# Kernel tuning notes

Measured on AMD Instinct MI355X. Metric: run time of the kernel, lower is better.

## Reference

```python
import jax, jax.numpy as jnp
import numpy as np

N_EMBD = 1024
N_HEAD = 16
HEAD_DIM = N_EMBD // N_HEAD


def setup_inputs() -> dict:
    key = jax.random.key(0)
    k1, k2, k3, k4, k5 = jax.random.split(key, 5)
    B, T, C = 4, 2048, N_EMBD
    s = 1.0 / np.sqrt(C)
    return {
        "x": jax.random.normal(k1, (B, T, C), dtype=jnp.float32),
        "W_attn": jax.random.normal(k2, (C, 3 * C), dtype=jnp.float32) * s,
        "b_attn": jnp.zeros((3 * C,), dtype=jnp.float32),
        "W_proj": jax.random.normal(k3, (C, C), dtype=jnp.float32) * s,
        "b_proj": jnp.zeros((C,), dtype=jnp.float32),
    }


def reference(x, W_attn, b_attn, W_proj, b_proj):
    B, T, C = x.shape
    H, D = N_HEAD, HEAD_DIM
    # fused QKV projection
    qkv = x @ W_attn + b_attn                       # [B,T,3C]
    q, k, v = jnp.split(qkv, 3, axis=2)
    q = q.reshape(B, T, H, D).transpose(0, 2, 1, 3)  # [B,H,T,D]
    k = k.reshape(B, T, H, D).transpose(0, 2, 1, 3)
    v = v.reshape(B, T, H, D).transpose(0, 2, 1, 3)
    # causal scaled dot-product attention
    scale = 1.0 / jnp.sqrt(jnp.asarray(D, dtype=x.dtype))
    scores = jnp.einsum('bhqd,bhkd->bhqk', q, k) * scale  # [B,H,T,T]
    causal = jnp.tril(jnp.ones((T, T), dtype=bool))
    scores = jnp.where(causal[None, None], scores, jnp.finfo(x.dtype).min)
    attn = jax.nn.softmax(scores, axis=-1)
    y = jnp.einsum('bhqk,bhkd->bhqd', attn, v)      # [B,H,T,D]
    y = y.transpose(0, 2, 1, 3).reshape(B, T, C)
    return y @ W_proj + b_proj
```

## Files before the change

kernel.cpp:

```cpp
#include <hip/hip_runtime.h>
#include <hip/hip_bf16.h>
#include <cstdint>

#define B_ 4
#define T_ 2048
#define C_ 1024
#define H_ 16
#define D_ 64
#define M_ (B_*T_)
#define N3 (3*C_)

typedef __bf16 bf16;
typedef __bf16 bf16x8 __attribute__((ext_vector_type(8)));
typedef __bf16 bf16x4 __attribute__((ext_vector_type(4)));
typedef float  floatx4 __attribute__((ext_vector_type(4)));

__device__ __forceinline__ void gl_lds16(const bf16* g, bf16* l) {
  __builtin_amdgcn_global_load_lds(
      (__attribute__((address_space(1))) void*)(void*)g,
      (__attribute__((address_space(3))) void*)(void*)l,
      16, 0, 0);
}

__device__ __forceinline__ uint32_t pack_bf16_trunc(float lo, float hi) {
  union { float f; uint32_t u; } a, b;
  a.f = lo; b.f = hi;
  return (a.u >> 16) | (b.u & 0xffff0000u);
}

__global__ void cast_to_bf16(const float* __restrict__ in, bf16* __restrict__ out, int n) {
  int i = (blockIdx.x * blockDim.x + threadIdx.x) * 4;
  if (i < n) {
    const float4 f = *(const float4*)(in + i);
    bf16x4 o;
    o.x = (bf16)f.x; o.y = (bf16)f.y; o.z = (bf16)f.z; o.w = (bf16)f.w;
    *(bf16x4*)(out + i) = o;
  }
}

__global__ void transpose_cast(const float* __restrict__ in, bf16* __restrict__ out,
                               int R, int C) {
  __shared__ float tile[32][33];
  int r0 = blockIdx.y * 32, c0 = blockIdx.x * 32;
  int tx = threadIdx.x & 31, ty = threadIdx.x >> 5;
  #pragma unroll
  for (int j = 0; j < 32; j += 8)
    tile[ty + j][tx] = in[(size_t)(r0 + ty + j) * C + c0 + tx];
  __syncthreads();
  #pragma unroll
  for (int j = 0; j < 32; j += 8)
    out[(size_t)(c0 + ty + j) * R + r0 + tx] = (bf16)tile[tx][ty + j];
}

__global__ __launch_bounds__(256)
void transpose_v(const bf16* __restrict__ in, bf16* __restrict__ out) {
  __shared__ __attribute__((aligned(16))) bf16 tileN[64 * 64];
  const int tid = threadIdx.x;
  const int bh = blockIdx.z;
  const int t0 = blockIdx.x * 64;
  const int sk = tid >> 2, scc = tid & 3;
  {
    const bf16* p = in + ((size_t)bh * T_ + t0 + sk) * D_ + scc * 16;
    const bf16x8 r0 = *(const bf16x8*)p;
    const bf16x8 r1 = *(const bf16x8*)(p + 8);
    *(bf16x8*)(tileN + sk * 64 + ((2 * scc)     ^ (sk & 7)) * 8) = r0;
    *(bf16x8*)(tileN + sk * 64 + ((2 * scc + 1) ^ (sk & 7)) * 8) = r1;
  }
  __syncthreads();
  const int tc = (tid & 7) * 8;
  #pragma unroll
  for (int half = 0; half < 2; half++) {
    const int d = (tid >> 3) + half * 32;
    bf16x8 o;
    #pragma unroll
    for (int j = 0; j < 8; j++) {
      const int slot = tc + j;
      const int row = 16 * (slot & 3) + (slot >> 2);
      o[j] = tileN[row * 64 + (((d >> 3) ^ (row & 7)) * 8) + (d & 7)];
    }
    *(bf16x8*)(out + ((size_t)bh * D_ + d) * T_ + t0 + tc) = o;
  }
}

template<int MODE>
__global__ __launch_bounds__(256)
void gemm_bt(const bf16* __restrict__ A, const bf16* __restrict__ Bt,
             const float* __restrict__ bias, float* __restrict__ out,
             bf16* __restrict__ qo, bf16* __restrict__ ko, bf16* __restrict__ vo,
             int M, int N, int K)
{
  __shared__ __attribute__((aligned(16))) bf16 As[128 * 32];
  __shared__ __attribute__((aligned(16))) bf16 Bs[128 * 32];

  const int tid  = threadIdx.x;
  const int w    = tid >> 6;
  const int lane = tid & 63;
  const int quad = lane >> 4;
  const int l16  = lane & 15;
  const int wm   = w & 1, wn = w >> 1;
  const int m0   = blockIdx.y * 128, n0 = blockIdx.x * 128;

  floatx4 acc[4][4] = {};

  const int lrow = lane >> 2;
  const int lk   = (lane & 3) * 8;

  const bf16* aptr = A  + (size_t)(m0 + w * 32 + lrow) * K + lk;
  const bf16* bptr = Bt + (size_t)(n0 + w * 32 + lrow) * K + lk;
  bf16* asl = As + w * 1024;
  bf16* bsl = Bs + w * 1024;

  for (int k0 = 0; k0 < K; k0 += 32) {
    gl_lds16(aptr,          asl);
    gl_lds16(aptr + 16 * K, asl + 512);
    gl_lds16(bptr,          bsl);
    gl_lds16(bptr + 16 * K, bsl + 512);
    aptr += 32; bptr += 32;
    __syncthreads();

    bf16x8 af[4], bfb[4];
    #pragma unroll
    for (int i = 0; i < 4; i++)
      af[i] = *(const bf16x8*)(As + (wm * 64 + i * 16 + l16) * 32 + quad * 8);
    #pragma unroll
    for (int i = 0; i < 4; i++)
      bfb[i] = *(const bf16x8*)(Bs + (wn * 64 + i * 16 + l16) * 32 + quad * 8);
    #pragma unroll
    for (int mi = 0; mi < 4; mi++)
      #pragma unroll
      for (int ni = 0; ni < 4; ni++)
        acc[mi][ni] = __builtin_amdgcn_mfma_f32_16x16x32_bf16(af[mi], bfb[ni], acc[mi][ni], 0, 0, 0);
    __syncthreads();
  }

  #pragma unroll
  for (int mi = 0; mi < 4; mi++) {
    #pragma unroll
    for (int ni = 0; ni < 4; ni++) {
      const int col = n0 + wn * 64 + ni * 16 + l16;
      const float bv = bias[col];
      #pragma unroll
      for (int r = 0; r < 4; r++) {
        const int row = m0 + wm * 64 + mi * 16 + quad * 4 + r;
        const float val = acc[mi][ni][r] + bv;
        if (MODE == 0) {
          const int b = row >> 11, t = row & 2047;
          const int s = col >> 10, c = col & 1023;
          const int h = c >> 6,  d = c & 63;
          bf16* dst = (s == 0) ? qo : (s == 1) ? ko : vo;
          dst[((size_t)(b * H_ + h) * T_ + t) * D_ + d] = (bf16)val;
        } else {
          out[(size_t)row * N + col] = val;
        }
      }
    }
  }
}

__global__ __launch_bounds__(256)
void attn_kernel(const bf16* __restrict__ Q, const bf16* __restrict__ Kp,
                 const bf16* __restrict__ Vtp, bf16* __restrict__ Y)
{
  __shared__ __attribute__((aligned(16))) bf16 Ks[2][64 * 72];
  __shared__ __attribute__((aligned(16))) bf16 Vs[2][64 * 72];
  __shared__ __attribute__((aligned(16))) bf16 Ps[4][16 * 72];

  const int tid  = threadIdx.x;
  const int w    = tid >> 6, lane = tid & 63;
  const int quad = lane >> 4, l16 = lane & 15;
  const int bh = blockIdx.x;
  const int b = bh >> 4, h = bh & 15;
  const int qt = 15 - (int)blockIdx.y;
  const int q0 = qt * 128;
  const int nch = 2 * qt + 2;

  const int sk = tid >> 2;
  const int sc = (tid & 3) * 16;

  const float SC = 0.125f * 1.44269504088896f;

  bf16x8 qf[2][2];
  #pragma unroll
  for (int mt = 0; mt < 2; mt++) {
    const bf16* qp = Q + ((size_t)bh * T_ + q0 + mt * 64 + w * 16 + l16) * D_ + quad * 8;
    qf[mt][0] = *(const bf16x8*)qp;
    qf[mt][1] = *(const bf16x8*)(qp + 32);
  }

  floatx4 o[2][4] = {};
  float l_r[2][4] = {};

  const bf16* kpp = Kp  + (size_t)bh * T_ * D_ + (size_t)sk * D_ + sc;
  const bf16* vpp = Vtp + (size_t)bh * D_ * T_ + (size_t)sk * T_ + sc;

  {
    const bf16x8 k0 = *(const bf16x8*)kpp, k1 = *(const bf16x8*)(kpp + 8);
    const bf16x8 v0 = *(const bf16x8*)vpp, v1 = *(const bf16x8*)(vpp + 8);
    bf16* kd = Ks[0] + sk * 72 + sc;
    *(bf16x8*)kd = k0; *(bf16x8*)(kd + 8) = k1;
    bf16* vd = Vs[0] + sk * 72 + sc;
    *(bf16x8*)vd = v0; *(bf16x8*)(vd + 8) = v1;
    kpp += 64 * D_; vpp += 64;
  }
  __syncthreads();

  #pragma unroll 1
  for (int c = 0; c < nch; c++) {
    const int cur = c & 1;

    bf16x8 nk0, nk1, nv0, nv1;
    const bool have = (c + 1 < nch);
    if (have) {
      nk0 = *(const bf16x8*)kpp; nk1 = *(const bf16x8*)(kpp + 8);
      nv0 = *(const bf16x8*)vpp; nv1 = *(const bf16x8*)(vpp + 8);
      kpp += 64 * D_; vpp += 64;
    }

    const bf16* KsC = Ks[cur];
    const bf16* VsC = Vs[cur];
    const int kv0 = c * 64;
    const bool act0 = (c < nch - 1);

    floatx4 s[2][4];
    #pragma unroll
    for (int nt = 0; nt < 4; nt++) {
      const bf16x8 kf0 = *(const bf16x8*)(KsC + (nt * 16 + l16) * 72 + quad * 8);
      const bf16x8 kf1 = *(const bf16x8*)(KsC + (nt * 16 + l16) * 72 + 32 + quad * 8);
      if (act0) {
        floatx4 z = {};
        z = __builtin_amdgcn_mfma_f32_16x16x32_bf16(qf[0][0], kf0, z, 0, 0, 0);
        s[0][nt] = __builtin_amdgcn_mfma_f32_16x16x32_bf16(qf[0][1], kf1, z, 0, 0, 0);
      }
      floatx4 z = {};
      z = __builtin_amdgcn_mfma_f32_16x16x32_bf16(qf[1][0], kf0, z, 0, 0, 0);
      s[1][nt] = __builtin_amdgcn_mfma_f32_16x16x32_bf16(qf[1][1], kf1, z, 0, 0, 0);
    }

    bf16x8 vfr[4][2];
    #pragma unroll
    for (int nt = 0; nt < 4; nt++) {
      vfr[nt][0] = *(const bf16x8*)(VsC + (nt * 16 + l16) * 72 + quad * 8);
      vfr[nt][1] = *(const bf16x8*)(VsC + (nt * 16 + l16) * 72 + 32 + quad * 8);
    }

    #pragma unroll
    for (int mt = 0; mt < 2; mt++) {
      if (mt == 0 && !act0) continue;
      const bool diag = (c == 2 * qt + mt);
      #pragma unroll
      for (int r = 0; r < 4; r++) {
        const int qrow = q0 + mt * 64 + w * 16 + quad * 4 + r;
        float x0 = s[mt][0][r], x1 = s[mt][1][r], x2 = s[mt][2][r], x3 = s[mt][3][r];
        if (diag) {
          if (kv0      + l16 > qrow) x0 = -1e30f;
          if (kv0 + 16 + l16 > qrow) x1 = -1e30f;
          if (kv0 + 32 + l16 > qrow) x2 = -1e30f;
          if (kv0 + 48 + l16 > qrow) x3 = -1e30f;
        }
        const float e0 = __builtin_amdgcn_exp2f(fmaf(x0, SC, -8.f));
        const float e1 = __builtin_amdgcn_exp2f(fmaf(x1, SC, -8.f));
        const float e2 = __builtin_amdgcn_exp2f(fmaf(x2, SC, -8.f));
        const float e3 = __builtin_amdgcn_exp2f(fmaf(x3, SC, -8.f));
        l_r[mt][r] += (e0 + e1) + (e2 + e3);
        uint2 pk;
        pk.x = pack_bf16_trunc(e0, e1);
        pk.y = pack_bf16_trunc(e2, e3);
        *(uint2*)(&Ps[w][(quad * 4 + r) * 72 + l16 * 4]) = pk;
      }
      const bf16x8 pf0 = *(const bf16x8*)(&Ps[w][l16 * 72 + quad * 8]);
      const bf16x8 pf1 = *(const bf16x8*)(&Ps[w][l16 * 72 + 32 + quad * 8]);
      #pragma unroll
      for (int nt = 0; nt < 4; nt++) {
        o[mt][nt] = __builtin_amdgcn_mfma_f32_16x16x32_bf16(pf0, vfr[nt][0], o[mt][nt], 0, 0, 0);
        o[mt][nt] = __builtin_amdgcn_mfma_f32_16x16x32_bf16(pf1, vfr[nt][1], o[mt][nt], 0, 0, 0);
      }
    }

    if (have) {
      bf16* kd = Ks[cur ^ 1] + sk * 72 + sc;
      *(bf16x8*)kd = nk0; *(bf16x8*)(kd + 8) = nk1;
      bf16* vd = Vs[cur ^ 1] + sk * 72 + sc;
      *(bf16x8*)vd = nv0; *(bf16x8*)(vd + 8) = nv1;
    }
    __syncthreads();
  }

  #pragma unroll
  for (int mt = 0; mt < 2; mt++) {
    #pragma unroll
    for (int r = 0; r < 4; r++) {
      float ls = l_r[mt][r];
      ls += __shfl_xor(ls, 1);
      ls += __shfl_xor(ls, 2);
      ls += __shfl_xor(ls, 4);
      ls += __shfl_xor(ls, 8);
      const float inv = 1.f / ls;
      const int t = q0 + mt * 64 + w * 16 + quad * 4 + r;
      #pragma unroll
      for (int nt = 0; nt < 4; nt++)
        Y[((size_t)b * T_ + t) * C_ + h * D_ + nt * 16 + l16] = (bf16)(o[mt][nt][r] * inv);
    }
  }
}

extern "C" void kernel_launch(void* const* d_in, const int* in_sizes, int n_in,
                              void* d_out, int out_size, void* d_ws, size_t ws_size,
                              hipStream_t stream)
{
  const float* x      = (const float*)d_in[0];
  const float* W_attn = (const float*)d_in[1];
  const float* b_attn = (const float*)d_in[2];
  const float* W_proj = (const float*)d_in[3];
  const float* b_proj = (const float*)d_in[4];
  float* out = (float*)d_out;

  bf16* xb  = (bf16*)d_ws;
  bf16* wat = xb  + (size_t)M_ * C_;
  bf16* wpt = wat + (size_t)N3 * C_;
  bf16* qb  = wpt + (size_t)C_ * C_;
  bf16* kb  = qb  + (size_t)M_ * C_;
  bf16* vb  = kb  + (size_t)M_ * C_;
  bf16* yb  = vb  + (size_t)M_ * C_;
  bf16* vtb = xb;

  cast_to_bf16<<<dim3(M_ * C_ / 1024), 256, 0, stream>>>(x, xb, M_ * C_);
  transpose_cast<<<dim3(N3 / 32, C_ / 32), 256, 0, stream>>>(W_attn, wat, C_, N3);
  transpose_cast<<<dim3(C_ / 32, C_ / 32), 256, 0, stream>>>(W_proj, wpt, C_, C_);
  gemm_bt<0><<<dim3(N3 / 128, M_ / 128), 256, 0, stream>>>(
      xb, wat, b_attn, nullptr, qb, kb, vb, M_, N3, C_);
  transpose_v<<<dim3(T_ / 64, 1, B_ * H_), 256, 0, stream>>>(vb, vtb);
  attn_kernel<<<dim3(B_ * H_, 16), 256, 0, stream>>>(qb, kb, vtb, yb);
  gemm_bt<1><<<dim3(C_ / 128, M_ / 128), 256, 0, stream>>>(
      yb, wpt, b_proj, out, nullptr, nullptr, nullptr, M_, C_, C_);
}
```

Measured before the change: 268.5 us.

## Fuse V transpose into QKV GEMM epilogue and vectorize GEMM output stores

The MFMA operand order is swapped so each lane's accumulator holds four consecutive output columns. The QKV and projection epilogues can then write bf16x4 and float4 vectors instead of scattered scalars. For the V slice, the epilogue writes directly into the permuted transposed layout that attention expects, so the separate transpose_v kernel and its round trip through memory go away. The cost is more complex epilogue indexing that must exactly match the token permutation the attention kernel assumes.

```diff
diff --git a/kernel.cpp b/kernel.cpp
--- a/kernel.cpp
+++ b/kernel.cpp
@@ -52,41 +52,11 @@
     out[(size_t)(c0 + ty + j) * R + r0 + tx] = (bf16)tile[tx][ty + j];
 }
 
-__global__ __launch_bounds__(256)
-void transpose_v(const bf16* __restrict__ in, bf16* __restrict__ out) {
-  __shared__ __attribute__((aligned(16))) bf16 tileN[64 * 64];
-  const int tid = threadIdx.x;
-  const int bh = blockIdx.z;
-  const int t0 = blockIdx.x * 64;
-  const int sk = tid >> 2, scc = tid & 3;
-  {
-    const bf16* p = in + ((size_t)bh * T_ + t0 + sk) * D_ + scc * 16;
-    const bf16x8 r0 = *(const bf16x8*)p;
-    const bf16x8 r1 = *(const bf16x8*)(p + 8);
-    *(bf16x8*)(tileN + sk * 64 + ((2 * scc)     ^ (sk & 7)) * 8) = r0;
-    *(bf16x8*)(tileN + sk * 64 + ((2 * scc + 1) ^ (sk & 7)) * 8) = r1;
-  }
-  __syncthreads();
-  const int tc = (tid & 7) * 8;
-  #pragma unroll
-  for (int half = 0; half < 2; half++) {
-    const int d = (tid >> 3) + half * 32;
-    bf16x8 o;
-    #pragma unroll
-    for (int j = 0; j < 8; j++) {
-      const int slot = tc + j;
-      const int row = 16 * (slot & 3) + (slot >> 2);
-      o[j] = tileN[row * 64 + (((d >> 3) ^ (row & 7)) * 8) + (d & 7)];
-    }
-    *(bf16x8*)(out + ((size_t)bh * D_ + d) * T_ + t0 + tc) = o;
-  }
-}
-
 template<int MODE>
 __global__ __launch_bounds__(256)
 void gemm_bt(const bf16* __restrict__ A, const bf16* __restrict__ Bt,
              const float* __restrict__ bias, float* __restrict__ out,
-             bf16* __restrict__ qo, bf16* __restrict__ ko, bf16* __restrict__ vo,
+             bf16* __restrict__ qo, bf16* __restrict__ ko, bf16* __restrict__ vtp,
              int M, int N, int K)
 {
   __shared__ __attribute__((aligned(16))) bf16 As[128 * 32];
@@ -126,32 +96,63 @@
     for (int i = 0; i < 4; i++)
       bfb[i] = *(const bf16x8*)(Bs + (wn * 64 + i * 16 + l16) * 32 + quad * 8);
     #pragma unroll
-    for (int mi = 0; mi < 4; mi++)
-      #pragma unroll
-      for (int ni = 0; ni < 4; ni++)
-        acc[mi][ni] = __builtin_amdgcn_mfma_f32_16x16x32_bf16(af[mi], bfb[ni], acc[mi][ni], 0, 0, 0);
+    for (int ni = 0; ni < 4; ni++)
+      #pragma unroll
+      for (int mi = 0; mi < 4; mi++)
+        acc[ni][mi] = __builtin_amdgcn_mfma_f32_16x16x32_bf16(bfb[ni], af[mi], acc[ni][mi], 0, 0, 0);
     __syncthreads();
   }
 
-  #pragma unroll
-  for (int mi = 0; mi < 4; mi++) {
+  if (MODE == 0) {
+    const int s   = n0 >> 10;
+    const int h   = ((n0 & 1023) >> 6) + wn;
+    const int b   = m0 >> 11;
+    const int t0w = (m0 & 2047) + wm * 64;
+    const size_t bh = (size_t)(b * H_ + h);
+    if (s < 2) {
+      bf16* dst = (s == 0) ? qo : ko;
+      #pragma unroll
+      for (int ni = 0; ni < 4; ni++) {
+        const float4 bv = *(const float4*)(bias + n0 + wn * 64 + ni * 16 + quad * 4);
+        #pragma unroll
+        for (int mi = 0; mi < 4; mi++) {
+          bf16x4 pv;
+          pv.x = (bf16)(acc[ni][mi][0] + bv.x);
+          pv.y = (bf16)(acc[ni][mi][1] + bv.y);
+          pv.z = (bf16)(acc[ni][mi][2] + bv.z);
+          pv.w = (bf16)(acc[ni][mi][3] + bv.w);
+          *(bf16x4*)(dst + (bh * T_ + t0w + mi * 16 + l16) * D_ + ni * 16 + quad * 4) = pv;
+        }
+      }
+    } else {
+      #pragma unroll
+      for (int ni = 0; ni < 4; ni++) {
+        const float4 bvv = *(const float4*)(bias + n0 + wn * 64 + ni * 16 + quad * 4);
+        const float bvr[4] = {bvv.x, bvv.y, bvv.z, bvv.w};
+        #pragma unroll
+        for (int r = 0; r < 4; r++) {
+          bf16x4 pv;
+          pv.x = (bf16)(acc[ni][0][r] + bvr[r]);
+          pv.y = (bf16)(acc[ni][1][r] + bvr[r]);
+          pv.z = (bf16)(acc[ni][2][r] + bvr[r]);
+          pv.w = (bf16)(acc[ni][3][r] + bvr[r]);
+          *(bf16x4*)(vtp + (bh * D_ + ni * 16 + quad * 4 + r) * T_ + t0w + 4 * l16) = pv;
+        }
+      }
+    }
+  } else {
     #pragma unroll
     for (int ni = 0; ni < 4; ni++) {
-      const int col = n0 + wn * 64 + ni * 16 + l16;
-      const float bv = bias[col];
-      #pragma unroll
-      for (int r = 0; r < 4; r++) {
-        const int row = m0 + wm * 64 + mi * 16 + quad * 4 + r;
-        const float val = acc[mi][ni][r] + bv;
-        if (MODE == 0) {
-          const int b = row >> 11, t = row & 2047;
-          const int s = col >> 10, c = col & 1023;
-          const int h = c >> 6,  d = c & 63;
-          bf16* dst = (s == 0) ? qo : (s == 1) ? ko : vo;
-          dst[((size_t)(b * H_ + h) * T_ + t) * D_ + d] = (bf16)val;
-        } else {
-          out[(size_t)row * N + col] = val;
-        }
+      const int col = n0 + wn * 64 + ni * 16 + quad * 4;
+      const float4 bv = *(const float4*)(bias + col);
+      #pragma unroll
+      for (int mi = 0; mi < 4; mi++) {
+        float4 v;
+        v.x = acc[ni][mi][0] + bv.x;
+        v.y = acc[ni][mi][1] + bv.y;
+        v.z = acc[ni][mi][2] + bv.z;
+        v.w = acc[ni][mi][3] + bv.w;
+        *(float4*)(out + (size_t)(m0 + wm * 64 + mi * 16 + l16) * N + col) = v;
       }
     }
   }
@@ -319,16 +320,14 @@
   bf16* wpt = wat + (size_t)N3 * C_;
   bf16* qb  = wpt + (size_t)C_ * C_;
   bf16* kb  = qb  + (size_t)M_ * C_;
-  bf16* vb  = kb  + (size_t)M_ * C_;
-  bf16* yb  = vb  + (size_t)M_ * C_;
-  bf16* vtb = xb;
+  bf16* vtb = kb  + (size_t)M_ * C_;
+  bf16* yb  = vtb + (size_t)M_ * C_;
 
   cast_to_bf16<<<dim3(M_ * C_ / 1024), 256, 0, stream>>>(x, xb, M_ * C_);
   transpose_cast<<<dim3(N3 / 32, C_ / 32), 256, 0, stream>>>(W_attn, wat, C_, N3);
   transpose_cast<<<dim3(C_ / 32, C_ / 32), 256, 0, stream>>>(W_proj, wpt, C_, C_);
   gemm_bt<0><<<dim3(N3 / 128, M_ / 128), 256, 0, stream>>>(
-      xb, wat, b_attn, nullptr, qb, kb, vb, M_, N3, C_);
-  transpose_v<<<dim3(T_ / 64, 1, B_ * H_), 256, 0, stream>>>(vb, vtb);
+      xb, wat, b_attn, nullptr, qb, kb, vtb, M_, N3, C_);
   attn_kernel<<<dim3(B_ * H_, 16), 256, 0, stream>>>(qb, kb, vtb, yb);
   gemm_bt<1><<<dim3(C_ / 128, M_ / 128), 256, 0, stream>>>(
       yb, wpt, b_proj, out, nullptr, nullptr, nullptr, M_, C_, C_);
```

Measured after the change: 283.3 us. 5.5% more time.
